# Optimization experiments

Hardware: AMD Instinct MI355X
Metric: run time of the kernel (lower is better)

The kernel has to match this reference:

```python
import jax, jax.numpy as jnp
import numpy as np

B, C, H, W = 1, 256, 48, 64
HW = H * W
HIDDEN, CTX = 128, 64
LEVELS, RADIUS = 4, 4
WIN = 2 * RADIUS + 1
P = WIN * WIN                     # 81 lookup points per level
CORR_DIM = P * LEVELS             # 324
TOP_K = 3
ITERS = 4
STEP_ROT, STEP_TRANS = 0.02, 0.02


def _sample_templates():
    # 12 directions x 3 scales + identity = 37 pose perturbations (as in __init__)
    base = [([0,0,0],[1,0,0]),([0,0,0],[-1,0,0]),([0,0,0],[0,1,0]),([0,0,0],[0,-1,0]),
            ([0,0,0],[0,0,1]),([0,0,0],[0,0,-1]),([1,0,0],[0,0,0]),([-1,0,0],[0,0,0]),
            ([0,1,0],[0,0,0]),([0,-1,0],[0,0,0]),([0,0,1],[0,0,0]),([0,0,-1],[0,0,0])]
    scales = np.array([0.25, 1.0, 4.0], np.float32)
    rot = np.repeat(np.array([r for r, _ in base], np.float32), 3, axis=0)
    trs = np.repeat(np.array([t for _, t in base], np.float32), 3, axis=0)
    sc = np.tile(scales, 12)
    axes = rot / np.clip(np.linalg.norm(rot, axis=1, keepdims=True), 1e-8, None)
    ha = STEP_ROT * sc / 2.0
    dq = np.stack([np.cos(ha), axes[:, 0]*np.sin(ha), axes[:, 1]*np.sin(ha), axes[:, 2]*np.sin(ha)], -1)
    dt = trs * (STEP_TRANS * sc[:, None])
    dq = np.concatenate([dq, [[1., 0., 0., 0.]]], 0)
    dt = np.concatenate([dt, [[0., 0., 0.]]], 0)
    return jnp.asarray(dq), jnp.asarray(dt)

DQ, DT = _sample_templates()     # (37,4), (37,3)
N_SAMPLES = DQ.shape[0]


def qmul(q, r):
    w1, x1, y1, z1 = jnp.moveaxis(q, -1, 0)
    w2, x2, y2, z2 = jnp.moveaxis(r, -1, 0)
    return jnp.stack([w1*w2 - x1*x2 - y1*y2 - z1*z2,
                      w1*x2 + x1*w2 + y1*z2 - z1*y2,
                      w1*y2 - x1*z2 + y1*w2 + z1*x2,
                      w1*z2 + x1*y2 - y1*x2 + z1*w2], -1)


def qapply(q, v):
    qv = jnp.concatenate([jnp.zeros(v.shape[:-1] + (1,), v.dtype), v], -1)
    qc = q * jnp.array([1., -1., -1., -1.], q.dtype)
    return qmul(qmul(q, qv), qc)[..., 1:]


def quat_to_R(q):
    w, x, y, z = jnp.moveaxis(q, -1, 0)
    R = jnp.stack([1-2*(y*y+z*z), 2*(x*y-w*z), 2*(x*z+w*y),
                   2*(x*y+w*z), 1-2*(x*x+z*z), 2*(y*z-w*x),
                   2*(x*z-w*y), 2*(y*z+w*x), 1-2*(x*x+y*y)], -1)
    return R.reshape(q.shape[:-1] + (3, 3))


def conv3(x, w, b):
    y = jax.lax.conv_general_dilated(x, w, (1, 1), 'SAME',
                                     dimension_numbers=('NCHW', 'OIHW', 'NCHW'))
    return y + b[None, :, None, None]


def bilinear_lookup(corr_flat, Hl, Wl, x, y):
    # corr_flat: (B,HW,Hl*Wl); x,y: (B,N,HW,P) -> (B,N,HW,P), zero padding outside
    x0 = jnp.floor(x)
    y0 = jnp.floor(y)
    out = jnp.zeros(x.shape, corr_flat.dtype)
    def gather(idx):
        g = lambda ix: jnp.take_along_axis(corr_flat, ix, axis=-1)
        return jax.vmap(g, in_axes=1, out_axes=1)(idx)   # vmap over N, no corr copy
    for dx_, dy_ in ((0, 0), (1, 0), (0, 1), (1, 1)):
        xi = x0 + dx_
        yi = y0 + dy_
        wgt = (1 - jnp.abs(x - xi)) * (1 - jnp.abs(y - yi))
        valid = (xi >= 0) & (xi < Wl) & (yi >= 0) & (yi < Hl)
        idx = (jnp.clip(yi, 0, Hl - 1) * Wl + jnp.clip(xi, 0, Wl - 1)).astype(jnp.int32)
        out = out + jnp.where(valid, wgt, 0.0) * gather(idx)
    return out


def _forward(fmap_rgb, fmap_depth, depth, context, intrinsics,
             Wz, bz, Wr, br, Wq, bq, Wh, bh, Wfc, bfc):
    f32 = jnp.float32
    fx = 60. + 40. * intrinsics[:, 0]
    fy = 60. + 40. * intrinsics[:, 1]
    cx = W / 2. + 4. * (intrinsics[:, 2] - 0.5)
    cy = H / 2. + 4. * (intrinsics[:, 3] - 0.5)
    d = 4.0 + 20.0 * depth                                  # (B,H,W) metric depth

    # 4D correlation pyramid: corr[b,i,:,:] = <fmap_depth pixel i, fmap_rgb>
    fd = fmap_depth.reshape(B, C, HW).transpose(0, 2, 1)    # (B,HW,C)
    corr = jnp.einsum('bic,bchw->bihw', fd, fmap_rgb) / jnp.sqrt(f32(C))
    pyramid = []
    cl, Hl, Wl = corr, H, W
    for _ in range(LEVELS):
        pyramid.append((cl.reshape(B, HW, Hl * Wl), Hl, Wl))
        cl = cl.reshape(B, HW, Hl // 2, 2, Wl // 2, 2).mean(axis=(3, 5))
        Hl //= 2
        Wl //= 2

    # back-projected depth points (B,HW,3)
    vv, uu = jnp.meshgrid(jnp.arange(H, dtype=f32), jnp.arange(W, dtype=f32), indexing='ij')
    uu = uu.reshape(HW)
    vv = vv.reshape(HW)
    df = d.reshape(B, HW)
    X = jnp.stack([(uu[None] - cx[:, None]) / fx[:, None] * df,
                   (vv[None] - cy[:, None]) / fy[:, None] * df, df], -1)

    off = jnp.arange(-RADIUS, RADIUS + 1, dtype=f32)
    oy, ox = jnp.meshgrid(off, off, indexing='ij')
    ox = ox.reshape(P)
    oy = oy.reshape(P)

    pose = jnp.tile(jnp.array([1., 0., 0., 0., 0., 0., 0.], f32)[None, :], (B, 1))
    h = jnp.zeros((B, HIDDEN, H, W), f32)

    for _ in range(ITERS):
        qc, tc = pose[:, :4], pose[:, 4:7]
        quats = qmul(qc[:, None, :], DQ[None])              # (B,N,4)
        quats = quats / jnp.linalg.norm(quats, axis=-1, keepdims=True)
        trans = tc[:, None, :] + qapply(qc[:, None, :], DT[None])
        Rm = quat_to_R(quats)                               # (B,N,3,3)
        Xc = jnp.einsum('bnij,bpj->bnpi', Rm, X) + trans[:, :, None, :]
        z = jnp.clip(Xc[..., 2], 0.1, None)
        u = fx[:, None, None] * Xc[..., 0] / z + cx[:, None, None]   # (B,N,HW)
        v = fy[:, None, None] * Xc[..., 1] / z + cy[:, None, None]
        feats = []
        for lvl, (cfl, Hl_, Wl_) in enumerate(pyramid):
            s = f32(2 ** lvl)
            xl = u[..., None] / s + ox
            yl = v[..., None] / s + oy
            feats.append(bilinear_lookup(cfl, Hl_, Wl_, xl, yl))
        cf = jnp.concatenate(feats, -1)                     # (B,N,HW,CORR_DIM)
        conf = cf.mean(axis=(2, 3))                         # (B,N) sample confidence
        topv, topi = jax.lax.top_k(conf, TOP_K)
        wk = jax.nn.softmax(topv, axis=-1)                  # confidence-weighted top-K
        idx = jnp.broadcast_to(topi[:, :, None, None], (B, TOP_K, HW, CORR_DIM))
        sel = jnp.take_along_axis(cf, idx, axis=1)
        fused = (wk[:, :, None, None] * sel).sum(1)         # (B,HW,CORR_DIM)
        fused = fused.transpose(0, 2, 1).reshape(B, CORR_DIM, H, W)

        # ConvGRU update
        x_in = jnp.concatenate([fused, context], 1)
        hx = jnp.concatenate([h, x_in], 1)
        zg = jax.nn.sigmoid(conv3(hx, Wz, bz))
        rg = jax.nn.sigmoid(conv3(hx, Wr, br))
        qg = jnp.tanh(conv3(jnp.concatenate([rg * h, x_in], 1), Wq, bq))
        h = (1 - zg) * h + zg * qg

        # 7D pose delta head + quaternion/Lie-style update
        feat = jax.nn.relu(conv3(h, Wh, bh)).mean(axis=(2, 3))
        delta = 0.01 * (feat @ Wfc + bfc)                   # (B,7)
        dq = jnp.concatenate([1.0 + delta[:, :1], delta[:, 1:4]], -1)
        dq = dq / jnp.linalg.norm(dq, axis=-1, keepdims=True)
        tn = tc + qapply(qc, delta[:, 4:7])
        qn = qmul(qc, dq)
        qn = qn / jnp.linalg.norm(qn, axis=-1, keepdims=True)
        pose = jnp.concatenate([qn, tn], -1)
    return pose


def setup_inputs() -> dict:
    key = jax.random.key(0)
    ks = jax.random.split(key, 12)
    rn = lambda k, shape, s=1.0: s * jax.random.normal(k, shape, jnp.float32)
    Gin = HIDDEN + CORR_DIM + CTX
    sc = 1.0 / np.sqrt(Gin * 9)
    sh = 1.0 / np.sqrt(HIDDEN * 9)
    return {
        'fmap_rgb': rn(ks[0], (B, C, H, W)),
        'fmap_depth': rn(ks[1], (B, C, H, W)),
        'depth': jax.random.uniform(ks[2], (B, H, W), jnp.float32),
        'context': rn(ks[3], (B, CTX, H, W)),
        'intrinsics': jax.random.uniform(ks[4], (B, 4), jnp.float32),
        'Wz': rn(ks[5], (HIDDEN, Gin, 3, 3), sc), 'bz': jnp.zeros((HIDDEN,), jnp.float32),
        'Wr': rn(ks[6], (HIDDEN, Gin, 3, 3), sc), 'br': jnp.zeros((HIDDEN,), jnp.float32),
        'Wq': rn(ks[7], (HIDDEN, Gin, 3, 3), sc), 'bq': jnp.zeros((HIDDEN,), jnp.float32),
        'Wh': rn(ks[8], (HIDDEN, HIDDEN, 3, 3), sh), 'bh': jnp.zeros((HIDDEN,), jnp.float32),
        'Wfc': rn(ks[9], (HIDDEN, 7), 1.0 / np.sqrt(HIDDEN)), 'bfc': jnp.zeros((7,), jnp.float32),
    }


def reference(fmap_rgb, fmap_depth, depth, context, intrinsics,
              Wz, bz, Wr, br, Wq, bq, Wh, bh, Wfc, bfc):
    return _forward(fmap_rgb, fmap_depth, depth, context, intrinsics,
                    Wz, bz, Wr, br, Wq, bq, Wh, bh, Wfc, bfc)
```

## Files before the change

### kernel.cpp

```cpp
#include <hip/hip_runtime.h>
#include <math.h>

constexpr int kH = 48, kW = 64, kHW = 3072, kC = 256;
constexpr int kHidden = 128, kCtx = 64;
constexpr int kP = 81, kCorrDim = 324;
constexpr int kNS = 37, kIters = 4;
constexpr int kGin = kHidden + kCorrDim + kCtx;
constexpr int kWp2 = 66, kHp2 = 50, kPix = 3300;
constexpr int kCF = 416;
constexpr int kCHh = 128;

constexpr int kSB0 = 0, kSB1 = 4292, kSB2 = 5720, kSB3 = 6292, kSBTot = 6580;
constexpr int kHB0 = 0, kHB1 = 3552, kHB2 = 4560, kHB3 = 4872, kHBTot = 4980;

constexpr size_t U_CORR0 = 0;
constexpr size_t U_CORR1 = U_CORR0 + (size_t)kHW * 3072;
constexpr size_t U_CORR2 = U_CORR1 + (size_t)kHW * 768;
constexpr size_t U_CORR3 = U_CORR2 + (size_t)kHW * 192;
constexpr size_t U_END0  = U_CORR3 + (size_t)kHW * 48;
constexpr size_t F_X     = U_END0 / 2;
constexpr size_t F_H     = F_X + (size_t)kHW * 3;
constexpr size_t F_ZPRE  = F_H + (size_t)kHidden * kHW;
constexpr size_t F_END1  = F_ZPRE + (size_t)kHidden * kHW;
constexpr size_t U_FCT   = F_END1 * 2;
constexpr size_t U_HT    = U_FCT + (size_t)kPix * kCF;
constexpr size_t U_RHT   = U_HT + (size_t)kPix * kCHh;
constexpr size_t U_PZR   = U_RHT + (size_t)kPix * kCHh;
constexpr size_t U_PQ    = U_PZR + (size_t)16 * 9 * 17 * 512;
constexpr size_t U_PH    = U_PQ + (size_t)8 * 9 * 17 * 512;
constexpr size_t U_END2  = U_PH + (size_t)8 * 9 * 4 * 512;
constexpr size_t F_BZR   = U_END2 / 2 + 1;
constexpr size_t F_CONF  = F_BZR + 256;
constexpr size_t F_POSE  = F_CONF + 64;
constexpr size_t F_FEAT  = F_POSE + 16;
constexpr size_t F_END3  = F_FEAT + 128;
constexpr size_t U_FDT   = F_END3 * 2;
constexpr size_t U_QT    = U_FDT + (size_t)kHW * kC;
constexpr size_t U_SBOX  = U_FDT;

typedef __attribute__((ext_vector_type(8))) short short8;
typedef __attribute__((ext_vector_type(4))) float f32x4;

__device__ inline unsigned short f2b(float f) {
  unsigned int u = __float_as_uint(f);
  unsigned int r = u + 0x7FFF + ((u >> 16) & 1);
  return (unsigned short)(r >> 16);
}
__device__ inline float b2f(unsigned short u) {
  return __uint_as_float(((unsigned int)u) << 16);
}
__device__ inline int clampi(int v, int lo, int hi) { return min(max(v, lo), hi); }

__constant__ float c_rot[12][3] = {
  {0,0,0},{0,0,0},{0,0,0},{0,0,0},{0,0,0},{0,0,0},
  {1,0,0},{-1,0,0},{0,1,0},{0,-1,0},{0,0,1},{0,0,-1}};
__constant__ float c_trs[12][3] = {
  {1,0,0},{-1,0,0},{0,1,0},{0,-1,0},{0,0,1},{0,0,-1},
  {0,0,0},{0,0,0},{0,0,0},{0,0,0},{0,0,0},{0,0,0}};

__device__ inline void d_qmul(const float* q, const float* r, float* o) {
  o[0] = q[0]*r[0] - q[1]*r[1] - q[2]*r[2] - q[3]*r[3];
  o[1] = q[0]*r[1] + q[1]*r[0] + q[2]*r[3] - q[3]*r[2];
  o[2] = q[0]*r[2] - q[1]*r[3] + q[2]*r[0] + q[3]*r[1];
  o[3] = q[0]*r[3] + q[1]*r[2] - q[2]*r[1] + q[3]*r[0];
}
__device__ inline void d_qapply(const float* q, const float* v, float* o) {
  float a0 = -q[1]*v[0] - q[2]*v[1] - q[3]*v[2];
  float a1 =  q[0]*v[0] + q[2]*v[2] - q[3]*v[1];
  float a2 =  q[0]*v[1] - q[1]*v[2] + q[3]*v[0];
  float a3 =  q[0]*v[2] + q[1]*v[1] - q[2]*v[0];
  o[0] = -a0*q[1] + a1*q[0] - a2*q[3] + a3*q[2];
  o[1] = -a0*q[2] + a1*q[3] + a2*q[0] - a3*q[1];
  o[2] = -a0*q[3] - a1*q[2] + a2*q[1] + a3*q[0];
}
__device__ inline void d_intr(const float* intr, float& fx, float& fy, float& cx, float& cy) {
  fx = 60.f + 40.f*intr[0];
  fy = 60.f + 40.f*intr[1];
  cx = 32.f + 4.f*(intr[2] - 0.5f);
  cy = 24.f + 4.f*(intr[3] - 0.5f);
}
__device__ inline void sample_Rt(int t, const float* __restrict__ pose, float* S) {
  float qc[4] = {pose[0], pose[1], pose[2], pose[3]};
  float tc[3] = {pose[4], pose[5], pose[6]};
  float dq[4], dt[3];
  if (t == 36) {
    dq[0] = 1.f; dq[1] = dq[2] = dq[3] = 0.f;
    dt[0] = dt[1] = dt[2] = 0.f;
  } else {
    int j = t / 3, k = t % 3;
    float sc = (k == 0) ? 0.25f : ((k == 1) ? 1.f : 4.f);
    float rx = c_rot[j][0], ry = c_rot[j][1], rz = c_rot[j][2];
    float nrm = sqrtf(rx*rx + ry*ry + rz*rz);
    float axn = fmaxf(nrm, 1e-8f);
    float ax = rx / axn, ay = ry / axn, az = rz / axn;
    float ha = 0.02f * sc * 0.5f;
    float sh = sinf(ha), ch = cosf(ha);
    dq[0] = ch; dq[1] = ax * sh; dq[2] = ay * sh; dq[3] = az * sh;
    dt[0] = c_trs[j][0] * (0.02f * sc);
    dt[1] = c_trs[j][1] * (0.02f * sc);
    dt[2] = c_trs[j][2] * (0.02f * sc);
  }
  float qn[4];
  d_qmul(qc, dq, qn);
  float inv = 1.f / sqrtf(qn[0]*qn[0] + qn[1]*qn[1] + qn[2]*qn[2] + qn[3]*qn[3]);
  qn[0] *= inv; qn[1] *= inv; qn[2] *= inv; qn[3] *= inv;
  float tr[3];
  d_qapply(qc, dt, tr);
  float w = qn[0], x = qn[1], y = qn[2], z = qn[3];
  S[0] = 1.f - 2.f*(y*y + z*z); S[1] = 2.f*(x*y - w*z);       S[2] = 2.f*(x*z + w*y);
  S[3] = 2.f*(x*y + w*z);       S[4] = 1.f - 2.f*(x*x + z*z); S[5] = 2.f*(y*z - w*x);
  S[6] = 2.f*(x*z - w*y);       S[7] = 2.f*(y*z + w*x);       S[8] = 1.f - 2.f*(x*x + y*y);
  S[9]  = tc[0] + tr[0];
  S[10] = tc[1] + tr[1];
  S[11] = tc[2] + tr[2];
}
__device__ inline void project_uv(const float* S, const float* Xp, const float* intr,
                                  float& u, float& v) {
  float xc0 = S[0]*Xp[0] + S[1]*Xp[1] + S[2]*Xp[2] + S[9];
  float xc1 = S[3]*Xp[0] + S[4]*Xp[1] + S[5]*Xp[2] + S[10];
  float xc2 = S[6]*Xp[0] + S[7]*Xp[1] + S[8]*Xp[2] + S[11];
  float z = fmaxf(xc2, 0.1f);
  float fx, fy, cx, cy;
  d_intr(intr, fx, fy, cx, cy);
  u = fx * xc0 / z + cx;
  v = fy * xc1 / z + cy;
}

__global__ void init_k(const float* __restrict__ ctx, const float* __restrict__ bz,
                       const float* __restrict__ br, const float* __restrict__ depth,
                       const float* __restrict__ intr, float* __restrict__ h,
                       unsigned int* __restrict__ zbase, unsigned short* __restrict__ fcT,
                       float* __restrict__ bzr, float* __restrict__ X,
                       float* __restrict__ conf, float* __restrict__ feat,
                       float* __restrict__ pose) {
  const size_t nz = ((size_t)kPix * (kCF + 2 * kCHh)) / 2;
  for (size_t i = blockIdx.x * blockDim.x + threadIdx.x; i < nz;
       i += (size_t)gridDim.x * blockDim.x)
    zbase[i] = 0;
  int idx = blockIdx.x * blockDim.x + threadIdx.x;
  if (idx < kHidden * kHW) h[idx] = 0.f;
  if (idx < kHW) {
    float fx, fy, cx, cy;
    d_intr(intr, fx, fy, cx, cy);
    float d = 4.f + 20.f * depth[idx];
    float u = (float)(idx % kW), v = (float)(idx / kW);
    X[idx*3+0] = (u - cx) / fx * d;
    X[idx*3+1] = (v - cy) / fy * d;
    X[idx*3+2] = d;
  }
  if (idx < 256) bzr[idx] = (idx < 128) ? bz[idx] : br[idx - 128];
  if (idx < 64) conf[idx] = 0.f;
  if (idx < 128) feat[idx] = 0.f;
  if (idx == 0) {
    pose[0] = 1.f;
    for (int j = 1; j < 7; ++j) pose[j] = 0.f;
  }
}
__global__ void initctx_k(const float* __restrict__ ctx, unsigned short* __restrict__ fcT) {
  int idx = blockIdx.x * blockDim.x + threadIdx.x;
  if (idx < kHW * 64) {
    int p = idx >> 6, c = idx & 63;
    int ppix = ((p >> 6) + 1) * kWp2 + (p & 63) + 1;
    fcT[(size_t)ppix * kCF + kCorrDim + c] = f2b(ctx[(size_t)c * kHW + p]);
  }
}

__global__ void pack_k(const float* __restrict__ W0, const float* __restrict__ W1,
                       int ocSplit, int OC, int NCH, int Cin,
                       unsigned short* __restrict__ P) {
  int idx = blockIdx.x * blockDim.x + threadIdx.x;
  int total = (OC / 16) * 9 * NCH * 64;
  if (idx >= total) return;
  int g = idx & 3;
  int m = (idx >> 2) & 15;
  int rest = idx >> 6;
  int cc = rest % NCH;
  int rest2 = rest / NCH;
  int tap = rest2 % 9;
  int ot = rest2 / 9;
  int oc = ot * 16 + m;
  union { unsigned short u[8]; uint4 q; } v;
#pragma unroll
  for (int j = 0; j < 8; ++j) {
    int ci = cc * 32 + g * 8 + j;
    float w = 0.f;
    if (ci < Cin)
      w = (oc < ocSplit) ? W0[((size_t)oc * Cin + ci) * 9 + tap]
                         : W1[((size_t)(oc - ocSplit) * Cin + ci) * 9 + tap];
    v.u[j] = f2b(w);
  }
  *(uint4*)&P[(size_t)idx * 8] = v.q;
}

__global__ __launch_bounds__(256) void t_bf16_k(const float* __restrict__ src,
                                                unsigned short* __restrict__ dst) {
  __shared__ float t[64][65];
  const int tid = threadIdx.x;
  const int p0 = blockIdx.x * 64, c0 = blockIdx.y * 64;
  const int tx = tid & 63, ty = tid >> 6;
  for (int cl = ty; cl < 64; cl += 4)
    t[cl][tx] = src[(size_t)(c0 + cl) * kHW + p0 + tx];
  __syncthreads();
  for (int pl = ty; pl < 64; pl += 4)
    dst[(size_t)(p0 + pl) * kC + c0 + tx] = f2b(t[tx][pl]);
}

__global__ __launch_bounds__(256) void corr_mfma_k(const unsigned short* __restrict__ fdT,
                                                   const unsigned short* __restrict__ qT,
                                                   unsigned short* __restrict__ Cg) {
  const int tid = threadIdx.x;
  const int wv = tid >> 6, lane = tid & 63;
  const int m = lane & 15, kg = lane >> 4;
  const int i0 = blockIdx.y * 128 + wv * 32;
  const int q0 = blockIdx.x * 128;

  f32x4 acc[2][8];
#pragma unroll
  for (int t = 0; t < 2; ++t)
#pragma unroll
    for (int u = 0; u < 8; ++u) acc[t][u] = (f32x4){0.f, 0.f, 0.f, 0.f};

#pragma unroll
  for (int kc = 0; kc < 8; ++kc) {
    const int kb = kc * 32 + kg * 8;
    short8 a[2], b[8];
#pragma unroll
    for (int t = 0; t < 2; ++t)
      a[t] = *(const short8*)&fdT[(size_t)(i0 + t * 16 + m) * kC + kb];
#pragma unroll
    for (int u = 0; u < 8; ++u)
      b[u] = *(const short8*)&qT[(size_t)(q0 + u * 16 + m) * kC + kb];
#pragma unroll
    for (int t = 0; t < 2; ++t)
#pragma unroll
      for (int u = 0; u < 8; ++u)
        acc[t][u] = __builtin_amdgcn_mfma_f32_16x16x32_bf16(a[t], b[u], acc[t][u], 0, 0, 0);
  }
  const float S = 0.0625f;
#pragma unroll
  for (int t = 0; t < 2; ++t)
#pragma unroll
    for (int u = 0; u < 8; ++u)
#pragma unroll
      for (int r = 0; r < 4; ++r)
        Cg[(size_t)(i0 + t * 16 + kg * 4 + r) * kHW + q0 + u * 16 + m] = f2b(acc[t][u][r] * S);
}

template<int HL>
__device__ inline void colpref(float* base, int Wp) {
  float v[HL];
#pragma unroll
  for (int y = 0; y < HL; ++y) v[y] = base[(size_t)y * Wp];
  float run = 0.f;
#pragma unroll
  for (int y = 0; y < HL; ++y) {
    run += v[y];
    base[(size_t)y * Wp] = run;
  }
}

__global__ __launch_bounds__(256) void boxbuild_k(const unsigned short* __restrict__ corr0,
                                                  unsigned short* __restrict__ corr1,
                                                  unsigned short* __restrict__ corr2,
                                                  unsigned short* __restrict__ corr3,
                                                  unsigned short* __restrict__ Sbox) {
  __shared__ float pyr[4080];
  __shared__ float hb[kHBTot];
  const int i = blockIdx.x;
  const int tid = threadIdx.x;
  const int wv = tid >> 6, lane = tid & 63;

  for (int idx = tid; idx < 3072; idx += 256)
    pyr[idx] = b2f(corr0[(size_t)i * 3072 + idx]);
  __syncthreads();

  for (int c = tid; c < 768; c += 256) {
    int y = c >> 5, x = c & 31;
    float v = 0.25f * (pyr[(2*y)*64 + 2*x] + pyr[(2*y)*64 + 2*x + 1] +
                       pyr[(2*y+1)*64 + 2*x] + pyr[(2*y+1)*64 + 2*x + 1]);
    unsigned short b = f2b(v);
    corr1[(size_t)i * 768 + c] = b;
    pyr[3072 + c] = b2f(b);
  }
  __syncthreads();
  for (int c = tid; c < 192; c += 256) {
    int y = c >> 4, x = c & 15;
    const float* p = pyr + 3072;
    float v = 0.25f * (p[(2*y)*32 + 2*x] + p[(2*y)*32 + 2*x + 1] +
                       p[(2*y+1)*32 + 2*x] + p[(2*y+1)*32 + 2*x + 1]);
    unsigned short b = f2b(v);
    corr2[(size_t)i * 192 + c] = b;
    pyr[3840 + c] = b2f(b);
  }
  __syncthreads();
  for (int c = tid; c < 48; c += 256) {
    int y = c >> 3, x = c & 7;
    const float* p = pyr + 3840;
    float v = 0.25f * (p[(2*y)*16 + 2*x] + p[(2*y)*16 + 2*x + 1] +
                       p[(2*y+1)*16 + 2*x] + p[(2*y+1)*16 + 2*x + 1]);
    unsigned short b = f2b(v);
    corr3[(size_t)i * 48 + c] = b;
    pyr[4032 + c] = b2f(b);
  }
  __syncthreads();

  const int lvl_off[4] = {0, 3072, 3840, 4032};
  for (int r = wv; r < 90; r += 4) {
    int lvl, y;
    if (r < 48)      { lvl = 0; y = r; }
    else if (r < 72) { lvl = 1; y = r - 48; }
    else if (r < 84) { lvl = 2; y = r - 72; }
    else             { lvl = 3; y = r - 84; }
    const int Wl = kW >> lvl;
    float* row = &pyr[lvl_off[lvl] + y * Wl];
    float v = (lane < Wl) ? row[lane] : 0.f;
#pragma unroll
    for (int o = 1; o < 64; o <<= 1) {
      float tv = __shfl_up(v, o, 64);
      if (lane >= o) v += tv;
    }
    if (lane < Wl) row[lane] = v;
  }
  __syncthreads();

  for (int c = tid; c < 3552; c += 256) {
    int y = c / 74, as = c % 74;
    const float* pref = &pyr[y * 64];
    float Hv = 0.f;
    if (as >= 1) Hv = pref[min(63, as - 1)];
    if (as >= 10) Hv -= pref[as - 10];
    hb[kHB0 + c] = Hv;
  }
  for (int c = tid; c < 1008; c += 256) {
    int y = c / 42, as = c % 42;
    const float* pref = &pyr[3072 + y * 32];
    float Hv = 0.f;
    if (as >= 1) Hv = pref[min(31, as - 1)];
    if (as >= 10) Hv -= pref[as - 10];
    hb[kHB1 + c] = Hv;
  }
  for (int c = tid; c < 312; c += 256) {
    int y = c / 26, as = c % 26;
    const float* pref = &pyr[3840 + y * 16];
    float Hv = 0.f;
    if (as >= 1) Hv = pref[min(15, as - 1)];
    if (as >= 10) Hv -= pref[as - 10];
    hb[kHB2 + c] = Hv;
  }
  for (int c = tid; c < 108; c += 256) {
    int y = c / 18, as = c % 18;
    const float* pref = &pyr[4032 + y * 8];
    float Hv = 0.f;
    if (as >= 1) Hv = pref[min(7, as - 1)];
    if (as >= 10) Hv -= pref[as - 10];
    hb[kHB3 + c] = Hv;
  }
  __syncthreads();

  if (tid < 160) {
    if (tid < 74)       colpref<48>(hb + kHB0 + tid, 74);
    else if (tid < 116) colpref<24>(hb + kHB1 + (tid - 74), 42);
    else if (tid < 142) colpref<12>(hb + kHB2 + (tid - 116), 26);
    else                colpref<6>(hb + kHB3 + (tid - 142), 18);
  }
  __syncthreads();

  unsigned short* out = Sbox + (size_t)i * kSBTot;
  for (int c = tid; c < 4292; c += 256) {
    int bp = c / 74, as = c % 74;
    const float* col = &hb[kHB0 + as];
    float S = 0.f;
    if (bp >= 1) S = col[min(47, bp - 1) * 74];
    if (bp >= 10) S -= col[(bp - 10) * 74];
    out[kSB0 + c] = f2b(S);
  }
  for (int c = tid; c < 1428; c += 256) {
    int bp = c / 42, as = c % 42;
    const float* col = &hb[kHB1 + as];
    float S = 0.f;
    if (bp >= 1) S = col[min(23, bp - 1) * 42];
    if (bp >= 10) S -= col[(bp - 10) * 42];
    out[kSB1 + c] = f2b(S);
  }
  for (int c = tid; c < 572; c += 256) {
    int bp = c / 26, as = c % 26;
    const float* col = &hb[kHB2 + as];
    float S = 0.f;
    if (bp >= 1) S = col[min(11, bp - 1) * 26];
    if (bp >= 10) S -= col[(bp - 10) * 26];
    out[kSB2 + c] = f2b(S);
  }
  for (int c = tid; c < 288; c += 256) {
    int bp = c / 18, as = c % 18;
    const float* col = &hb[kHB3 + as];
    float S = 0.f;
    if (bp >= 1) S = col[min(5, bp - 1) * 18];
    if (bp >= 10) S -= col[(bp - 10) * 18];
    out[kSB3 + c] = f2b(S);
  }
}

__global__ __launch_bounds__(256) void conf_k(const unsigned short* __restrict__ Sbox,
                                              const float* __restrict__ X,
                                              const float* __restrict__ pose,
                                              const float* __restrict__ intr,
                                              float* __restrict__ conf) {
  const int idx = blockIdx.x * 256 + threadIdx.x;
  const int n = idx / kHW, i = idx - n * kHW;
  float S[12];
  sample_Rt(n, pose, S);
  float Xp[3] = {X[i*3], X[i*3+1], X[i*3+2]};
  float u, v;
  project_uv(S, Xp, intr, u, v);
  const unsigned short* sb = Sbox + (size_t)i * kSBTot;
  float tot = 0.f;
#pragma unroll
  for (int l = 0; l < 4; ++l) {
    const int Wp = (kW >> l) + 10, Hp = (kH >> l) + 10;
    const int so = (l == 0) ? kSB0 : (l == 1) ? kSB1 : (l == 2) ? kSB2 : kSB3;
    const float s = (float)(1 << l);
    const float bx = u / s, by = v / s;
    const float fbx = floorf(bx), fby = floorf(by);
    const int x0 = (int)fbx, y0 = (int)fby;
    const float fx = bx - fbx, fy = by - fby;
    const int xa = clampi(x0 + 5, 0, Wp - 1), xb = clampi(x0 + 6, 0, Wp - 1);
    const int ya = clampi(y0 + 5, 0, Hp - 1), yb = clampi(y0 + 6, 0, Hp - 1);
    const float s00 = b2f(sb[so + ya * Wp + xa]), s10 = b2f(sb[so + ya * Wp + xb]);
    const float s01 = b2f(sb[so + yb * Wp + xa]), s11 = b2f(sb[so + yb * Wp + xb]);
    tot += (1.f - fx) * (1.f - fy) * s00 + fx * (1.f - fy) * s10 +
           (1.f - fx) * fy * s01 + fx * fy * s11;
  }
#pragma unroll
  for (int o = 32; o; o >>= 1) tot += __shfl_xor(tot, o, 64);
  if ((threadIdx.x & 63) == 0) atomicAdd(&conf[n], tot);
}

__global__ __launch_bounds__(256) void fused_k(const unsigned short* __restrict__ corr0,
                                               const unsigned short* __restrict__ corr1,
                                               const unsigned short* __restrict__ corr2,
                                               const unsigned short* __restrict__ corr3,
                                               const float* __restrict__ X,
                                               const float* __restrict__ pose,
                                               const float* __restrict__ intr,
                                               const float* __restrict__ conf,
                                               unsigned short* __restrict__ fcT) {
  __shared__ float win[12][10][12];
  __shared__ float s_fx[12], s_fy[12];
  __shared__ int   s_ix[12], s_iy[12];
  __shared__ float s_w[3];
  __shared__ int   s_id[3];
  const int i = blockIdx.x;
  const int tid = threadIdx.x;

  if (tid == 0) {
    const float scale = 1.f / ((float)kHW * (float)kCorrDim);
    float c[kNS];
    for (int n = 0; n < kNS; ++n) c[n] = conf[n] * scale;
    int id[3] = {-1, -1, -1};
    float v[3];
    for (int k = 0; k < 3; ++k) {
      float best = -1e30f;
      int bi = -1;
      for (int n = 0; n < kNS; ++n) {
        if (n == id[0] || n == id[1] || n == id[2]) continue;
        if (c[n] > best) { best = c[n]; bi = n; }
      }
      v[k] = best;
      id[k] = bi;
    }
    float m = v[0];
    float e0 = expf(v[0] - m), e1 = expf(v[1] - m), e2 = expf(v[2] - m);
    float s = e0 + e1 + e2;
    s_w[0] = e0 / s; s_w[1] = e1 / s; s_w[2] = e2 / s;
    s_id[0] = id[0]; s_id[1] = id[1]; s_id[2] = id[2];
  }
  __syncthreads();

  if (tid < 3) {
    int n = s_id[tid];
    float S[12];
    sample_Rt(n, pose, S);
    float Xp[3] = {X[i*3], X[i*3+1], X[i*3+2]};
    float u, v;
    project_uv(S, Xp, intr, u, v);
#pragma unroll
    for (int l = 0; l < 4; ++l) {
      float s = (float)(1 << l);
      float bx = u / s, by = v / s;
      float fbx = floorf(bx), fby = floorf(by);
      s_ix[tid*4 + l] = (int)fbx;
      s_iy[tid*4 + l] = (int)fby;
      s_fx[tid*4 + l] = bx - fbx;
      s_fy[tid*4 + l] = by - fby;
    }
  }
  __syncthreads();

  for (int sidx = tid; sidx < 1200; sidx += 256) {
    const int w = sidx / 100, rem = sidx % 100;
    const int rr = rem / 10, cc = rem % 10;
    const int lvl = w & 3;
    const int Wl = kW >> lvl, Hl = kH >> lvl;
    const unsigned short* base =
        (lvl == 0) ? corr0 : (lvl == 1) ? corr1 : (lvl == 2) ? corr2 : corr3;
    const int y = s_iy[w] - 4 + rr;
    const int x = s_ix[w] - 4 + cc;
    float v = 0.f;
    if (y >= 0 && y < Hl && x >= 0 && x < Wl)
      v = b2f(base[(size_t)i * (Hl * Wl) + y * Wl + x]);
    win[w][rr][cc] = v;
  }
  __syncthreads();

  const int ppix = ((i >> 6) + 1) * kWp2 + (i & 63) + 1;
  for (int d = tid; d < kCorrDim; d += 256) {
    const int lvl = d / kP;
    const int o = d % kP;
    const int oyi = o / 9, oxi = o % 9;
    float val = 0.f;
#pragma unroll
    for (int k = 0; k < 3; ++k) {
      const int w = k * 4 + lvl;
      const float fx = s_fx[w], fy = s_fy[w];
      const float w00 = (1.f - fx) * (1.f - fy), w10 = fx * (1.f - fy);
      const float w01 = (1.f - fx) * fy, w11 = fx * fy;
      val += s_w[k] * (w00 * win[w][oyi][oxi] + w10 * win[w][oyi][oxi + 1] +
                       w01 * win[w][oyi + 1][oxi] + w11 * win[w][oyi + 1][oxi + 1]);
    }
    fcT[(size_t)ppix * kCF + d] = f2b(val);
  }
}

template<int CCB, int CCE, int NCHH, int NCHTOT>
__device__ inline void conv_core32(const unsigned short* __restrict__ srcH,
                                   const unsigned short* __restrict__ srcF,
                                   const unsigned short* __restrict__ A,
                                   int y, int xbase, int ot, int lane,
                                   f32x4 (&acc)[2]) {
  const int m = lane & 15, kg = lane >> 4;
  const unsigned short* a_base = A + (size_t)ot * (9 * NCHTOT * 512) + m * 32 + kg * 8;
  const int pix0 = (y + 1) * kWp2 + (xbase + 1) + m;
#pragma unroll
  for (int tap = 0; tap < 9; ++tap) {
    const int dy = tap / 3 - 1, dx = tap % 3 - 1;
    const int po = pix0 + dy * kWp2 + dx;
    const unsigned short* bh0 = srcH + (size_t)po * kCHh + kg * 8;
    const unsigned short* bf0 = srcF + (size_t)po * kCF + kg * 8;
#pragma unroll
    for (int cc = CCB; cc < CCE; ++cc) {
      const int s = tap * NCHTOT + cc;
      short8 a = *(const short8*)(a_base + (size_t)s * 512);
      short8 b0, b1;
      if (cc < NCHH) {
        b0 = *(const short8*)(bh0 + cc * 32);
        b1 = *(const short8*)(bh0 + 16 * kCHh + cc * 32);
      } else {
        b0 = *(const short8*)(bf0 + (cc - NCHH) * 32);
        b1 = *(const short8*)(bf0 + 16 * kCF + (cc - NCHH) * 32);
      }
      acc[0] = __builtin_amdgcn_mfma_f32_16x16x32_bf16(a, b0, acc[0], 0, 0, 0);
      acc[1] = __builtin_amdgcn_mfma_f32_16x16x32_bf16(a, b1, acc[1], 0, 0, 0);
    }
  }
}

__global__ __launch_bounds__(256) void conv_zr_k(const unsigned short* __restrict__ hT,
                                                 const unsigned short* __restrict__ fcT,
                                                 const unsigned short* __restrict__ P,
                                                 const float* __restrict__ bzr,
                                                 float* __restrict__ zpre,
                                                 const float* __restrict__ hbuf,
                                                 unsigned short* __restrict__ rhT) {
  __shared__ f32x4 red[2][2][64];
  const int tid = threadIdx.x;
  const int wv = tid >> 6, lane = tid & 63;
  const int p = wv >> 1, half = wv & 1;
  const int y = blockIdx.y >> 1, xbase = (blockIdx.y & 1) * 32;
  const int ot = blockIdx.x * 2 + p;
  f32x4 acc[2] = {{0.f,0.f,0.f,0.f},{0.f,0.f,0.f,0.f}};
  if (half == 0) conv_core32<0, 9, 4, 17>(hT, fcT, P, y, xbase, ot, lane, acc);
  else           conv_core32<9, 17, 4, 17>(hT, fcT, P, y, xbase, ot, lane, acc);
  if (half == 1) {
    red[p][0][lane] = acc[0];
    red[p][1][lane] = acc[1];
  }
  __syncthreads();
  if (half != 0) return;
  acc[0] += red[p][0][lane];
  acc[1] += red[p][1][lane];
  const int m = lane & 15, kg = lane >> 4;
#pragma unroll
  for (int t = 0; t < 2; ++t)
#pragma unroll
    for (int r = 0; r < 4; ++r) {
      const int oc = ot * 16 + kg * 4 + r;
      const int pxx = xbase + t * 16 + m;
      const int px = y * kW + pxx;
      const float val = acc[t][r] + bzr[oc];
      if (oc < kHidden) {
        zpre[(size_t)oc * kHW + px] = val;
      } else {
        const float rg = 1.f / (1.f + expf(-val));
        const int ppix = (y + 1) * kWp2 + pxx + 1;
        rhT[(size_t)ppix * kCHh + oc - kHidden] =
            f2b(rg * hbuf[(size_t)(oc - kHidden) * kHW + px]);
      }
    }
}

__global__ __launch_bounds__(256) void conv_q_k(const unsigned short* __restrict__ rhT,
                                                const unsigned short* __restrict__ fcT,
                                                unsigned short* __restrict__ hT,
                                                const unsigned short* __restrict__ P,
                                                const float* __restrict__ bq,
                                                const float* __restrict__ zpre,
                                                float* __restrict__ hbuf) {
  __shared__ f32x4 red[2][2][64];
  const int tid = threadIdx.x;
  const int wv = tid >> 6, lane = tid & 63;
  const int p = wv >> 1, half = wv & 1;
  const int y = blockIdx.y >> 1, xbase = (blockIdx.y & 1) * 32;
  const int ot = blockIdx.x * 2 + p;
  f32x4 acc[2] = {{0.f,0.f,0.f,0.f},{0.f,0.f,0.f,0.f}};
  if (half == 0) conv_core32<0, 9, 4, 17>(rhT, fcT, P, y, xbase, ot, lane, acc);
  else           conv_core32<9, 17, 4, 17>(rhT, fcT, P, y, xbase, ot, lane, acc);
  if (half == 1) {
    red[p][0][lane] = acc[0];
    red[p][1][lane] = acc[1];
  }
  __syncthreads();
  if (half != 0) return;
  acc[0] += red[p][0][lane];
  acc[1] += red[p][1][lane];
  const int m = lane & 15, kg = lane >> 4;
#pragma unroll
  for (int t = 0; t < 2; ++t)
#pragma unroll
    for (int r = 0; r < 4; ++r) {
      const int oc = ot * 16 + kg * 4 + r;
      const int pxx = xbase + t * 16 + m;
      const int px = y * kW + pxx;
      const size_t off = (size_t)oc * kHW + px;
      const float q = acc[t][r] + bq[oc];
      const float zg = 1.f / (1.f + expf(-zpre[off]));
      const float hn = (1.f - zg) * hbuf[off] + zg * tanhf(q);
      hbuf[off] = hn;
      const int ppix = (y + 1) * kWp2 + pxx + 1;
      hT[(size_t)ppix * kCHh + oc] = f2b(hn);
    }
}

__global__ __launch_bounds__(256) void conv_h_k(const unsigned short* __restrict__ hT,
                                                const unsigned short* __restrict__ P,
                                                const float* __restrict__ bh,
                                                float* __restrict__ feat) {
  const int tid = threadIdx.x;
  const int wv = tid >> 6, lane = tid & 63;
  const int y = blockIdx.y >> 1, xbase = (blockIdx.y & 1) * 32;
  const int ot = blockIdx.x * 4 + wv;
  f32x4 acc[2] = {{0.f,0.f,0.f,0.f},{0.f,0.f,0.f,0.f}};
  conv_core32<0, 4, 4, 4>(hT, hT, P, y, xbase, ot, lane, acc);
  const int m = lane & 15, kg = lane >> 4;
#pragma unroll
  for (int r = 0; r < 4; ++r) {
    const int oc = ot * 16 + kg * 4 + r;
    const float bv = bh[oc];
    float v = fmaxf(acc[0][r] + bv, 0.f) + fmaxf(acc[1][r] + bv, 0.f);
    v += __shfl_xor(v, 1, 64);
    v += __shfl_xor(v, 2, 64);
    v += __shfl_xor(v, 4, 64);
    v += __shfl_xor(v, 8, 64);
    if (m == 0) atomicAdd(&feat[oc], v);
  }
}

__global__ void pose_update_k(float* __restrict__ feat, float* __restrict__ conf,
                              const float* __restrict__ Wfc,
                              const float* __restrict__ bfc, float* __restrict__ pose,
                              float* __restrict__ out) {
  __shared__ float s_d[7];
  int t = threadIdx.x;
  if (t < 7) {
    float s = 0.f;
    const float inv = 1.f / (float)kHW;
    for (int k = 0; k < kHidden; ++k) s += (feat[k] * inv) * Wfc[k * 7 + t];
    s_d[t] = 0.01f * (s + bfc[t]);
  }
  __syncthreads();
  if (t < kHidden) feat[t] = 0.f;
  if (t < 64) conf[t] = 0.f;
  if (t != 0) return;
  float qc[4] = {pose[0], pose[1], pose[2], pose[3]};
  float tc[3] = {pose[4], pose[5], pose[6]};
  float dq[4] = {1.f + s_d[0], s_d[1], s_d[2], s_d[3]};
  float inv = 1.f / sqrtf(dq[0]*dq[0] + dq[1]*dq[1] + dq[2]*dq[2] + dq[3]*dq[3]);
  dq[0] *= inv; dq[1] *= inv; dq[2] *= inv; dq[3] *= inv;
  float dv[3] = {s_d[4], s_d[5], s_d[6]};
  float rv[3];
  d_qapply(qc, dv, rv);
  float tn[3] = {tc[0] + rv[0], tc[1] + rv[1], tc[2] + rv[2]};
  float qn[4];
  d_qmul(qc, dq, qn);
  float inv2 = 1.f / sqrtf(qn[0]*qn[0] + qn[1]*qn[1] + qn[2]*qn[2] + qn[3]*qn[3]);
  qn[0] *= inv2; qn[1] *= inv2; qn[2] *= inv2; qn[3] *= inv2;
  pose[0] = qn[0]; pose[1] = qn[1]; pose[2] = qn[2]; pose[3] = qn[3];
  pose[4] = tn[0]; pose[5] = tn[1]; pose[6] = tn[2];
  out[0] = qn[0]; out[1] = qn[1]; out[2] = qn[2]; out[3] = qn[3];
  out[4] = tn[0]; out[5] = tn[1]; out[6] = tn[2];
}

extern "C" void kernel_launch(void* const* d_in, const int* in_sizes, int n_in,
                              void* d_out, int out_size, void* d_ws, size_t ws_size,
                              hipStream_t stream) {
  const float* frgb  = (const float*)d_in[0];
  const float* fdep  = (const float*)d_in[1];
  const float* depth = (const float*)d_in[2];
  const float* ctx   = (const float*)d_in[3];
  const float* intr  = (const float*)d_in[4];
  const float* Wz = (const float*)d_in[5];
  const float* bz = (const float*)d_in[6];
  const float* Wr = (const float*)d_in[7];
  const float* br = (const float*)d_in[8];
  const float* Wq = (const float*)d_in[9];
  const float* bq = (const float*)d_in[10];
  const float* Wh = (const float*)d_in[11];
  const float* bh = (const float*)d_in[12];
  const float* Wfc = (const float*)d_in[13];
  const float* bfc = (const float*)d_in[14];
  float* outp = (float*)d_out;

  float* ws = (float*)d_ws;
  unsigned short* us = (unsigned short*)d_ws;
  unsigned short* corr0 = us + U_CORR0;
  unsigned short* corr1 = us + U_CORR1;
  unsigned short* corr2 = us + U_CORR2;
  unsigned short* corr3 = us + U_CORR3;
  float* X    = ws + F_X;
  float* hbuf = ws + F_H;
  float* zpre = ws + F_ZPRE;
  unsigned short* fcT = us + U_FCT;
  unsigned short* hT  = us + U_HT;
  unsigned short* rhT = us + U_RHT;
  unsigned short* Pzr = us + U_PZR;
  unsigned short* Pq  = us + U_PQ;
  unsigned short* Ph  = us + U_PH;
  float* bzr  = ws + F_BZR;
  float* conf = ws + F_CONF;
  float* pose = ws + F_POSE;
  float* feat = ws + F_FEAT;
  unsigned short* fdT  = us + U_FDT;
  unsigned short* qT   = us + U_QT;
  unsigned short* Sbox = us + U_SBOX;

  init_k<<<1536, 256, 0, stream>>>(ctx, bz, br, depth, intr, hbuf,
                                   (unsigned int*)fcT, fcT, bzr, X, conf, feat, pose);
  initctx_k<<<768, 256, 0, stream>>>(ctx, fcT);
  pack_k<<<(16 * 9 * 17 * 64 + 255) / 256, 256, 0, stream>>>(Wz, Wr, 128, 256, 17,
                                                             kGin, Pzr);
  pack_k<<<(8 * 9 * 17 * 64 + 255) / 256, 256, 0, stream>>>(Wq, Wq, 128, 128, 17,
                                                            kGin, Pq);
  pack_k<<<(8 * 9 * 4 * 64 + 255) / 256, 256, 0, stream>>>(Wh, Wh, 128, 128, 4,
                                                           kHidden, Ph);
  t_bf16_k<<<dim3(48, 4), 256, 0, stream>>>(fdep, fdT);
  t_bf16_k<<<dim3(48, 4), 256, 0, stream>>>(frgb, qT);
  corr_mfma_k<<<dim3(24, 24), 256, 0, stream>>>(fdT, qT, corr0);
  boxbuild_k<<<kHW, 256, 0, stream>>>(corr0, corr1, corr2, corr3, Sbox);

  for (int it = 0; it < kIters; ++it) {
    conf_k<<<444, 256, 0, stream>>>(Sbox, X, pose, intr, conf);
    fused_k<<<kHW, 256, 0, stream>>>(corr0, corr1, corr2, corr3, X, pose, intr,
                                     conf, fcT);
    conv_zr_k<<<dim3(8, 96), 256, 0, stream>>>(hT, fcT, Pzr, bzr, zpre, hbuf, rhT);
    conv_q_k<<<dim3(4, 96), 256, 0, stream>>>(rhT, fcT, hT, Pq, bq, zpre, hbuf);
    conv_h_k<<<dim3(2, 96), 256, 0, stream>>>(hT, Ph, bh, feat);
    pose_update_k<<<1, 128, 0, stream>>>(feat, conf, Wfc, bfc, pose, outp);
  }
}
```

Baseline: 821.9 us.

## Precompute sample poses once per iteration and split conv K-loop across more waves

Pose-sample rotation/translation matrices are now computed once in pose_update_k (and init_k) and stored in a small buffer. conf_k and fused_k read them instead of recomputing sample_Rt in every thread. The three GRU convolutions split their channel-chunk loop over more waves, reduced through shared memory, and launch twice as many blocks to raise parallelism. The cost is extra shared-memory reductions and idle waves during the final reduction.

```diff
diff --git a/kernel.cpp b/kernel.cpp
--- a/kernel.cpp
+++ b/kernel.cpp
@@ -33,7 +33,8 @@
 constexpr size_t F_CONF  = F_BZR + 256;
 constexpr size_t F_POSE  = F_CONF + 64;
 constexpr size_t F_FEAT  = F_POSE + 16;
-constexpr size_t F_END3  = F_FEAT + 128;
+constexpr size_t F_SAMP  = F_FEAT + 128;
+constexpr size_t F_END3  = F_SAMP + 448;
 constexpr size_t U_FDT   = F_END3 * 2;
 constexpr size_t U_QT    = U_FDT + (size_t)kHW * kC;
 constexpr size_t U_SBOX  = U_FDT;
@@ -132,7 +133,7 @@
                        unsigned int* __restrict__ zbase, unsigned short* __restrict__ fcT,
                        float* __restrict__ bzr, float* __restrict__ X,
                        float* __restrict__ conf, float* __restrict__ feat,
-                       float* __restrict__ pose) {
+                       float* __restrict__ pose, float* __restrict__ samp) {
   const size_t nz = ((size_t)kPix * (kCF + 2 * kCHh)) / 2;
   for (size_t i = blockIdx.x * blockDim.x + threadIdx.x; i < nz;
        i += (size_t)gridDim.x * blockDim.x)
@@ -151,6 +152,10 @@
   if (idx < 256) bzr[idx] = (idx < 128) ? bz[idx] : br[idx - 128];
   if (idx < 64) conf[idx] = 0.f;
   if (idx < 128) feat[idx] = 0.f;
+  if (idx < kNS) {
+    const float ipose[7] = {1.f, 0.f, 0.f, 0.f, 0.f, 0.f, 0.f};
+    sample_Rt(idx, ipose, samp + idx * 12);
+  }
   if (idx == 0) {
     pose[0] = 1.f;
     for (int j = 1; j < 7; ++j) pose[j] = 0.f;
@@ -402,13 +407,12 @@
 
 __global__ __launch_bounds__(256) void conf_k(const unsigned short* __restrict__ Sbox,
                                               const float* __restrict__ X,
-                                              const float* __restrict__ pose,
+                                              const float* __restrict__ samp,
                                               const float* __restrict__ intr,
                                               float* __restrict__ conf) {
   const int idx = blockIdx.x * 256 + threadIdx.x;
   const int n = idx / kHW, i = idx - n * kHW;
-  float S[12];
-  sample_Rt(n, pose, S);
+  const float* S = samp + n * 12;
   float Xp[3] = {X[i*3], X[i*3+1], X[i*3+2]};
   float u, v;
   project_uv(S, Xp, intr, u, v);
@@ -440,7 +444,7 @@
                                                const unsigned short* __restrict__ corr2,
                                                const unsigned short* __restrict__ corr3,
                                                const float* __restrict__ X,
-                                               const float* __restrict__ pose,
+                                               const float* __restrict__ samp,
                                                const float* __restrict__ intr,
                                                const float* __restrict__ conf,
                                                unsigned short* __restrict__ fcT) {
@@ -477,9 +481,7 @@
   __syncthreads();
 
   if (tid < 3) {
-    int n = s_id[tid];
-    float S[12];
-    sample_Rt(n, pose, S);
+    const float* S = samp + s_id[tid] * 12;
     float Xp[3] = {X[i*3], X[i*3+1], X[i*3+2]};
     float u, v;
     project_uv(S, Xp, intr, u, v);
@@ -571,23 +573,27 @@
                                                  float* __restrict__ zpre,
                                                  const float* __restrict__ hbuf,
                                                  unsigned short* __restrict__ rhT) {
-  __shared__ f32x4 red[2][2][64];
+  __shared__ f32x4 red[3][2][64];
   const int tid = threadIdx.x;
   const int wv = tid >> 6, lane = tid & 63;
-  const int p = wv >> 1, half = wv & 1;
   const int y = blockIdx.y >> 1, xbase = (blockIdx.y & 1) * 32;
-  const int ot = blockIdx.x * 2 + p;
+  const int ot = blockIdx.x;
   f32x4 acc[2] = {{0.f,0.f,0.f,0.f},{0.f,0.f,0.f,0.f}};
-  if (half == 0) conv_core32<0, 9, 4, 17>(hT, fcT, P, y, xbase, ot, lane, acc);
-  else           conv_core32<9, 17, 4, 17>(hT, fcT, P, y, xbase, ot, lane, acc);
-  if (half == 1) {
-    red[p][0][lane] = acc[0];
-    red[p][1][lane] = acc[1];
-  }
-  __syncthreads();
-  if (half != 0) return;
-  acc[0] += red[p][0][lane];
-  acc[1] += red[p][1][lane];
+  if (wv == 0)      conv_core32<0, 5, 4, 17>(hT, fcT, P, y, xbase, ot, lane, acc);
+  else if (wv == 1) conv_core32<5, 9, 4, 17>(hT, fcT, P, y, xbase, ot, lane, acc);
+  else if (wv == 2) conv_core32<9, 13, 4, 17>(hT, fcT, P, y, xbase, ot, lane, acc);
+  else              conv_core32<13, 17, 4, 17>(hT, fcT, P, y, xbase, ot, lane, acc);
+  if (wv != 0) {
+    red[wv - 1][0][lane] = acc[0];
+    red[wv - 1][1][lane] = acc[1];
+  }
+  __syncthreads();
+  if (wv != 0) return;
+#pragma unroll
+  for (int j = 0; j < 3; ++j) {
+    acc[0] += red[j][0][lane];
+    acc[1] += red[j][1][lane];
+  }
   const int m = lane & 15, kg = lane >> 4;
 #pragma unroll
   for (int t = 0; t < 2; ++t)
@@ -615,23 +621,27 @@
                                                 const float* __restrict__ bq,
                                                 const float* __restrict__ zpre,
                                                 float* __restrict__ hbuf) {
-  __shared__ f32x4 red[2][2][64];
+  __shared__ f32x4 red[3][2][64];
   const int tid = threadIdx.x;
   const int wv = tid >> 6, lane = tid & 63;
-  const int p = wv >> 1, half = wv & 1;
   const int y = blockIdx.y >> 1, xbase = (blockIdx.y & 1) * 32;
-  const int ot = blockIdx.x * 2 + p;
+  const int ot = blockIdx.x;
   f32x4 acc[2] = {{0.f,0.f,0.f,0.f},{0.f,0.f,0.f,0.f}};
-  if (half == 0) conv_core32<0, 9, 4, 17>(rhT, fcT, P, y, xbase, ot, lane, acc);
-  else           conv_core32<9, 17, 4, 17>(rhT, fcT, P, y, xbase, ot, lane, acc);
-  if (half == 1) {
-    red[p][0][lane] = acc[0];
-    red[p][1][lane] = acc[1];
-  }
-  __syncthreads();
-  if (half != 0) return;
-  acc[0] += red[p][0][lane];
-  acc[1] += red[p][1][lane];
+  if (wv == 0)      conv_core32<0, 5, 4, 17>(rhT, fcT, P, y, xbase, ot, lane, acc);
+  else if (wv == 1) conv_core32<5, 9, 4, 17>(rhT, fcT, P, y, xbase, ot, lane, acc);
+  else if (wv == 2) conv_core32<9, 13, 4, 17>(rhT, fcT, P, y, xbase, ot, lane, acc);
+  else              conv_core32<13, 17, 4, 17>(rhT, fcT, P, y, xbase, ot, lane, acc);
+  if (wv != 0) {
+    red[wv - 1][0][lane] = acc[0];
+    red[wv - 1][1][lane] = acc[1];
+  }
+  __syncthreads();
+  if (wv != 0) return;
+#pragma unroll
+  for (int j = 0; j < 3; ++j) {
+    acc[0] += red[j][0][lane];
+    acc[1] += red[j][1][lane];
+  }
   const int m = lane & 15, kg = lane >> 4;
 #pragma unroll
   for (int t = 0; t < 2; ++t)
@@ -654,12 +664,23 @@
                                                 const unsigned short* __restrict__ P,
                                                 const float* __restrict__ bh,
                                                 float* __restrict__ feat) {
+  __shared__ f32x4 red[2][2][64];
   const int tid = threadIdx.x;
   const int wv = tid >> 6, lane = tid & 63;
+  const int p = wv >> 1, half = wv & 1;
   const int y = blockIdx.y >> 1, xbase = (blockIdx.y & 1) * 32;
-  const int ot = blockIdx.x * 4 + wv;
+  const int ot = blockIdx.x * 2 + p;
   f32x4 acc[2] = {{0.f,0.f,0.f,0.f},{0.f,0.f,0.f,0.f}};
-  conv_core32<0, 4, 4, 4>(hT, hT, P, y, xbase, ot, lane, acc);
+  if (half == 0) conv_core32<0, 2, 4, 4>(hT, hT, P, y, xbase, ot, lane, acc);
+  else           conv_core32<2, 4, 4, 4>(hT, hT, P, y, xbase, ot, lane, acc);
+  if (half == 1) {
+    red[p][0][lane] = acc[0];
+    red[p][1][lane] = acc[1];
+  }
+  __syncthreads();
+  if (half != 0) return;
+  acc[0] += red[p][0][lane];
+  acc[1] += red[p][1][lane];
   const int m = lane & 15, kg = lane >> 4;
 #pragma unroll
   for (int r = 0; r < 4; ++r) {
@@ -677,8 +698,9 @@
 __global__ void pose_update_k(float* __restrict__ feat, float* __restrict__ conf,
                               const float* __restrict__ Wfc,
                               const float* __restrict__ bfc, float* __restrict__ pose,
-                              float* __restrict__ out) {
+                              float* __restrict__ samp, float* __restrict__ out) {
   __shared__ float s_d[7];
+  __shared__ float s_pose[7];
   int t = threadIdx.x;
   if (t < 7) {
     float s = 0.f;
@@ -689,24 +711,29 @@
   __syncthreads();
   if (t < kHidden) feat[t] = 0.f;
   if (t < 64) conf[t] = 0.f;
-  if (t != 0) return;
-  float qc[4] = {pose[0], pose[1], pose[2], pose[3]};
-  float tc[3] = {pose[4], pose[5], pose[6]};
-  float dq[4] = {1.f + s_d[0], s_d[1], s_d[2], s_d[3]};
-  float inv = 1.f / sqrtf(dq[0]*dq[0] + dq[1]*dq[1] + dq[2]*dq[2] + dq[3]*dq[3]);
-  dq[0] *= inv; dq[1] *= inv; dq[2] *= inv; dq[3] *= inv;
-  float dv[3] = {s_d[4], s_d[5], s_d[6]};
-  float rv[3];
-  d_qapply(qc, dv, rv);
-  float tn[3] = {tc[0] + rv[0], tc[1] + rv[1], tc[2] + rv[2]};
-  float qn[4];
-  d_qmul(qc, dq, qn);
-  float inv2 = 1.f / sqrtf(qn[0]*qn[0] + qn[1]*qn[1] + qn[2]*qn[2] + qn[3]*qn[3]);
-  qn[0] *= inv2; qn[1] *= inv2; qn[2] *= inv2; qn[3] *= inv2;
-  pose[0] = qn[0]; pose[1] = qn[1]; pose[2] = qn[2]; pose[3] = qn[3];
-  pose[4] = tn[0]; pose[5] = tn[1]; pose[6] = tn[2];
-  out[0] = qn[0]; out[1] = qn[1]; out[2] = qn[2]; out[3] = qn[3];
-  out[4] = tn[0]; out[5] = tn[1]; out[6] = tn[2];
+  if (t == 0) {
+    float qc[4] = {pose[0], pose[1], pose[2], pose[3]};
+    float tc[3] = {pose[4], pose[5], pose[6]};
+    float dq[4] = {1.f + s_d[0], s_d[1], s_d[2], s_d[3]};
+    float inv = 1.f / sqrtf(dq[0]*dq[0] + dq[1]*dq[1] + dq[2]*dq[2] + dq[3]*dq[3]);
+    dq[0] *= inv; dq[1] *= inv; dq[2] *= inv; dq[3] *= inv;
+    float dv[3] = {s_d[4], s_d[5], s_d[6]};
+    float rv[3];
+    d_qapply(qc, dv, rv);
+    float tn[3] = {tc[0] + rv[0], tc[1] + rv[1], tc[2] + rv[2]};
+    float qn[4];
+    d_qmul(qc, dq, qn);
+    float inv2 = 1.f / sqrtf(qn[0]*qn[0] + qn[1]*qn[1] + qn[2]*qn[2] + qn[3]*qn[3]);
+    qn[0] *= inv2; qn[1] *= inv2; qn[2] *= inv2; qn[3] *= inv2;
+    s_pose[0] = qn[0]; s_pose[1] = qn[1]; s_pose[2] = qn[2]; s_pose[3] = qn[3];
+    s_pose[4] = tn[0]; s_pose[5] = tn[1]; s_pose[6] = tn[2];
+    pose[0] = qn[0]; pose[1] = qn[1]; pose[2] = qn[2]; pose[3] = qn[3];
+    pose[4] = tn[0]; pose[5] = tn[1]; pose[6] = tn[2];
+    out[0] = qn[0]; out[1] = qn[1]; out[2] = qn[2]; out[3] = qn[3];
+    out[4] = tn[0]; out[5] = tn[1]; out[6] = tn[2];
+  }
+  __syncthreads();
+  if (t < kNS) sample_Rt(t, s_pose, samp + t * 12);
 }
 
 extern "C" void kernel_launch(void* const* d_in, const int* in_sizes, int n_in,
@@ -748,12 +775,14 @@
   float* conf = ws + F_CONF;
   float* pose = ws + F_POSE;
   float* feat = ws + F_FEAT;
+  float* samp = ws + F_SAMP;
   unsigned short* fdT  = us + U_FDT;
   unsigned short* qT   = us + U_QT;
   unsigned short* Sbox = us + U_SBOX;
 
   init_k<<<1536, 256, 0, stream>>>(ctx, bz, br, depth, intr, hbuf,
-                                   (unsigned int*)fcT, fcT, bzr, X, conf, feat, pose);
+                                   (unsigned int*)fcT, fcT, bzr, X, conf, feat,
+                                   pose, samp);
   initctx_k<<<768, 256, 0, stream>>>(ctx, fcT);
   pack_k<<<(16 * 9 * 17 * 64 + 255) / 256, 256, 0, stream>>>(Wz, Wr, 128, 256, 17,
                                                              kGin, Pzr);
@@ -767,12 +796,12 @@
   boxbuild_k<<<kHW, 256, 0, stream>>>(corr0, corr1, corr2, corr3, Sbox);
 
   for (int it = 0; it < kIters; ++it) {
-    conf_k<<<444, 256, 0, stream>>>(Sbox, X, pose, intr, conf);
-    fused_k<<<kHW, 256, 0, stream>>>(corr0, corr1, corr2, corr3, X, pose, intr,
+    conf_k<<<444, 256, 0, stream>>>(Sbox, X, samp, intr, conf);
+    fused_k<<<kHW, 256, 0, stream>>>(corr0, corr1, corr2, corr3, X, samp, intr,
                                      conf, fcT);
-    conv_zr_k<<<dim3(8, 96), 256, 0, stream>>>(hT, fcT, Pzr, bzr, zpre, hbuf, rhT);
-    conv_q_k<<<dim3(4, 96), 256, 0, stream>>>(rhT, fcT, hT, Pq, bq, zpre, hbuf);
-    conv_h_k<<<dim3(2, 96), 256, 0, stream>>>(hT, Ph, bh, feat);
-    pose_update_k<<<1, 128, 0, stream>>>(feat, conf, Wfc, bfc, pose, outp);
-  }
-}
+    conv_zr_k<<<dim3(16, 96), 256, 0, stream>>>(hT, fcT, Pzr, bzr, zpre, hbuf, rhT);
+    conv_q_k<<<dim3(8, 96), 256, 0, stream>>>(rhT, fcT, hT, Pq, bq, zpre, hbuf);
+    conv_h_k<<<dim3(4, 96), 256, 0, stream>>>(hT, Ph, bh, feat);
+    pose_update_k<<<1, 128, 0, stream>>>(feat, conf, Wfc, bfc, pose, samp, outp);
+  }
+}
```

Result: faster. 775.8 us (median of 2 runs) (-5.6%).
